# Optimization experiments

Hardware: AMD Instinct MI355X
Metric: run time of the kernel (lower is better)

## Reference

```python
import jax, jax.numpy as jnp
import numpy as np

N = 16384          # num nodes (128 graphs x 128 turbines)
E = 262144         # edges before self loops
TURBINE_NUM = 128
D_IN = 512         # input_dim (= 2*hidden_dim1)
H1 = 256           # hidden_dim1
H2 = 256           # hidden_dim2
NEG_SLOPE = 0.2    # PyG GATConv default leaky relu slope


def _glorot(key, shape, fan_in):
    return jax.random.normal(key, shape, dtype=jnp.float32) / np.sqrt(fan_in)


def setup_inputs() -> dict:
    key = jax.random.key(0)
    ks = jax.random.split(key, 12)
    x = jax.random.normal(ks[0], (N, H2), dtype=jnp.float32)
    adj = jax.random.randint(ks[1], (2, E), 0, N, dtype=jnp.int64)
    # fc: Linear(hidden_dim2 -> hidden_dim1); stored as [in, out]
    W_fc = _glorot(ks[2], (H2, H1), H2)
    b_fc = jnp.zeros((H1,), dtype=jnp.float32)
    # gat1: GATConv(H1 -> H1, heads=2, concat)
    W1 = _glorot(ks[3], (H1, 2 * H1), H1)
    a1_src = _glorot(ks[4], (2, H1), H1)
    a1_dst = _glorot(ks[5], (2, H1), H1)
    b1 = jnp.zeros((2 * H1,), dtype=jnp.float32)
    # gat2: GATConv(D_IN -> D_IN, heads=1, concat)
    W2 = _glorot(ks[6], (D_IN, D_IN), D_IN)
    a2_src = _glorot(ks[7], (1, D_IN), D_IN)
    a2_dst = _glorot(ks[8], (1, D_IN), D_IN)
    b2 = jnp.zeros((D_IN,), dtype=jnp.float32)
    return dict(x=x, adj=adj, W_fc=W_fc, b_fc=b_fc, W1=W1, a1_src=a1_src,
                a1_dst=a1_dst, b1=b1, W2=W2, a2_src=a2_src, a2_dst=a2_dst, b2=b2)


def gat_conv(x, src, dst, W, a_src, a_dst, bias, heads, out_ch):
    """PyG GATConv (eval mode, self loops already in src/dst)."""
    n = x.shape[0]
    h = (x @ W).reshape(n, heads, out_ch)                 # [N,H,C]
    al_s = jnp.einsum('nhc,hc->nh', h, a_src)             # [N,H]
    al_d = jnp.einsum('nhc,hc->nh', h, a_dst)
    e = jax.nn.leaky_relu(al_s[src] + al_d[dst], NEG_SLOPE)  # [E,H]
    # segment softmax over incoming edges per destination node
    e_max = jax.ops.segment_max(e, dst, num_segments=n)
    e_exp = jnp.exp(e - e_max[dst])
    denom = jax.ops.segment_sum(e_exp, dst, num_segments=n)
    alpha = e_exp / (denom[dst] + 1e-16)                  # [E,H]
    msg = h[src] * alpha[:, :, None]                      # [E,H,C]
    out = jax.ops.segment_sum(msg, dst, num_segments=n)   # [N,H,C]
    return out.reshape(n, heads * out_ch) + bias


def reference(x, adj, W_fc, b_fc, W1, a1_src, a1_dst, b1, W2, a2_src, a2_dst, b2):
    # add self loops (PyG GATConv default)
    loops = jnp.arange(N, dtype=adj.dtype)
    src = jnp.concatenate([adj[0], loops])
    dst = jnp.concatenate([adj[1], loops])
    h = jax.nn.relu(x @ W_fc + b_fc)                      # fc + ReLU
    h = gat_conv(h, src, dst, W1, a1_src, a1_dst, b1, heads=2, out_ch=H1)
    h = jax.nn.relu(h)
    h = gat_conv(h, src, dst, W2, a2_src, a2_dst, b2, heads=1, out_ch=D_IN)
    y = jax.nn.relu(h)
    return y.reshape(-1, TURBINE_NUM, y.shape[1])         # [128,128,512]
```

## Files before the change

kernel.cpp:

```cpp
#include <hip/hip_runtime.h>

#define N_NODES 16384
#define N_EDGES 262144
#define E_TOT   (N_EDGES + N_NODES)
#define NEG_SLOPE 0.2f

typedef __attribute__((ext_vector_type(8))) short short8;
typedef __attribute__((ext_vector_type(4))) float floatx4;
typedef __attribute__((ext_vector_type(2))) float floatx2;
typedef __attribute__((ext_vector_type(4))) int intx4;

__device__ __forceinline__ float bf2f(ushort u) {
    return __uint_as_float(((unsigned)u) << 16);
}
__device__ __forceinline__ ushort f2bf(float f) {
    unsigned u = __float_as_uint(f);
    u += 0x7fffu + ((u >> 16) & 1u);
    return (ushort)(u >> 16);
}
__device__ __forceinline__ float leaky(float x) {
    return x > 0.f ? x : NEG_SLOPE * x;
}

#define PREP_CAST   524288
#define PREP_T0     (PREP_CAST)
#define PREP_T1     (PREP_T0 + 65536)
#define PREP_T2     (PREP_T1 + 131072)
#define PREP_Z      (PREP_T2 + 262144)
#define PREP_TOT    (PREP_Z + 4096)

__global__ __launch_bounds__(256) void k_prep(const float* __restrict__ x,
                                              ushort* __restrict__ xb,
                                              const float* __restrict__ Wfc,
                                              ushort* __restrict__ WfcT,
                                              const float* __restrict__ W1,
                                              ushort* __restrict__ W1T,
                                              const float* __restrict__ W2,
                                              ushort* __restrict__ W2T,
                                              int* __restrict__ counts) {
    int idx = blockIdx.x * 256 + threadIdx.x;
    if (idx < PREP_CAST) {
        floatx4 v0 = *(const floatx4*)(x + (size_t)idx * 8);
        floatx4 v1 = *(const floatx4*)(x + (size_t)idx * 8 + 4);
        short8 r;
        r[0] = (short)f2bf(v0[0]); r[1] = (short)f2bf(v0[1]);
        r[2] = (short)f2bf(v0[2]); r[3] = (short)f2bf(v0[3]);
        r[4] = (short)f2bf(v1[0]); r[5] = (short)f2bf(v1[1]);
        r[6] = (short)f2bf(v1[2]); r[7] = (short)f2bf(v1[3]);
        *(short8*)(xb + (size_t)idx * 8) = r;
    } else if (idx < PREP_T1) {
        int t = idx - PREP_T0;
        int k = t >> 8, n = t & 255;
        WfcT[n * 256 + k] = f2bf(Wfc[t]);
    } else if (idx < PREP_T2) {
        int t = idx - PREP_T1;
        int k = t >> 9, n = t & 511;
        W1T[n * 256 + k] = f2bf(W1[t]);
    } else if (idx < PREP_Z) {
        int t = idx - PREP_T2;
        int k = t >> 9, n = t & 511;
        W2T[n * 512 + k] = f2bf(W2[t]);
    } else if (idx < PREP_TOT) {
        int t = idx - PREP_Z;
        *(intx4*)(counts + t * 4) = (intx4){0, 0, 0, 0};
    }
}

__global__ __launch_bounds__(256) void k_hist(const int* __restrict__ adj,
                                              int* __restrict__ counts) {
    int e = blockIdx.x * 256 + threadIdx.x;
    if (e < E_TOT) {
        int d = (e < N_EDGES) ? adj[N_EDGES + e] : (e - N_EDGES);
        atomicAdd(&counts[d], 1);
    }
}

__global__ __launch_bounds__(1024) void k_scan(const int* __restrict__ counts,
                                               int* __restrict__ offs,
                                               int* __restrict__ cursor) {
    __shared__ int part[1024];
    int t = threadIdx.x;
    int local[16];
    int sum = 0;
#pragma unroll
    for (int i = 0; i < 16; i++) {
        local[i] = sum;
        sum += counts[t * 16 + i];
    }
    part[t] = sum;
    __syncthreads();
    for (int d = 1; d < 1024; d <<= 1) {
        int v = (t >= d) ? part[t - d] : 0;
        __syncthreads();
        part[t] += v;
        __syncthreads();
    }
    int base = (t == 0) ? 0 : part[t - 1];
#pragma unroll
    for (int i = 0; i < 16; i++) {
        int o = base + local[i];
        offs[t * 16 + i] = o;
        cursor[t * 16 + i] = o;
    }
    if (t == 1023) offs[N_NODES] = part[1023];
}

__global__ __launch_bounds__(256) void k_scatter(const int* __restrict__ adj,
                                                 int* __restrict__ cursor,
                                                 int* __restrict__ esrc) {
    int e = blockIdx.x * 256 + threadIdx.x;
    if (e < E_TOT) {
        int s, d;
        if (e < N_EDGES) { s = adj[e]; d = adj[N_EDGES + e]; }
        else             { s = e - N_EDGES; d = s; }
        int pos = atomicAdd(&cursor[d], 1);
        esrc[pos] = s;
    }
}

#define BM 64
#define BN 64
#define BK 64
#define LDK (BK + 8)

__global__ __launch_bounds__(256) void gemm_bt(const ushort* __restrict__ A,
                                               const ushort* __restrict__ BT,
                                               const float* __restrict__ bias,
                                               ushort* __restrict__ C,
                                               int M, int Nc, int K, int relu) {
    __shared__ ushort As[BM * LDK];
    __shared__ ushort Bs[BN * LDK];
    int tid  = threadIdx.x;
    int wave = tid >> 6, lane = tid & 63;
    int quad = lane >> 4, l16 = lane & 15;
    int bm = blockIdx.x * BM, bn = blockIdx.y * BN;

    floatx4 acc[4];
#pragma unroll
    for (int j = 0; j < 4; j++) acc[j] = (floatx4){0.f, 0.f, 0.f, 0.f};

    int srow = tid >> 3;
    int skc  = (tid & 7) * 8;

    for (int kb = 0; kb < K; kb += BK) {
        const ushort* ga = A + (size_t)(bm + srow) * K + kb + skc;
        short8 a0 = *(const short8*)ga;
        short8 a1 = *(const short8*)(ga + (size_t)32 * K);
        const ushort* gb = BT + (size_t)(bn + srow) * K + kb + skc;
        short8 b0 = *(const short8*)gb;
        short8 b1 = *(const short8*)(gb + (size_t)32 * K);
        *(short8*)&As[srow * LDK + skc] = a0;
        *(short8*)&As[(srow + 32) * LDK + skc] = a1;
        *(short8*)&Bs[srow * LDK + skc] = b0;
        *(short8*)&Bs[(srow + 32) * LDK + skc] = b1;
        __syncthreads();

        int arow = wave * 16 + l16;
#pragma unroll
        for (int kk = 0; kk < BK; kk += 32) {
            short8 a = *(const short8*)&As[arow * LDK + kk + quad * 8];
#pragma unroll
            for (int j4 = 0; j4 < 4; j4++) {
                short8 b = *(const short8*)&Bs[(j4 * 16 + l16) * LDK + kk + quad * 8];
                acc[j4] = __builtin_amdgcn_mfma_f32_16x16x32_bf16(a, b, acc[j4], 0, 0, 0);
            }
        }
        __syncthreads();
    }

    int row = bm + wave * 16 + quad * 4;
#pragma unroll
    for (int j4 = 0; j4 < 4; j4++) {
        int col = bn + j4 * 16 + l16;
        float bv = bias ? bias[col] : 0.f;
#pragma unroll
        for (int i = 0; i < 4; i++) {
            float v = acc[j4][i] + bv;
            if (relu) v = fmaxf(v, 0.f);
            C[(size_t)(row + i) * Nc + col] = f2bf(v);
        }
    }
}

__global__ __launch_bounds__(256) void k_dots(const ushort* __restrict__ h,
                                              const float* __restrict__ asrc,
                                              const float* __restrict__ adst,
                                              float* __restrict__ als,
                                              float* __restrict__ ald,
                                              int heads) {
    int wave = threadIdx.x >> 6, lane = threadIdx.x & 63;
    int n = blockIdx.x * 4 + wave;
    const ushort* hr = h + (size_t)n * 512;
    int c = lane * 8;
    short8 hv = *(const short8*)(hr + c);
    floatx4 s0 = *(const floatx4*)(asrc + c);
    floatx4 s1 = *(const floatx4*)(asrc + c + 4);
    floatx4 d0 = *(const floatx4*)(adst + c);
    floatx4 d1 = *(const floatx4*)(adst + c + 4);
    float ps = 0.f, pd = 0.f;
#pragma unroll
    for (int j = 0; j < 4; j++) {
        float hf0 = bf2f((ushort)hv[j]);
        float hf1 = bf2f((ushort)hv[j + 4]);
        ps += hf0 * s0[j] + hf1 * s1[j];
        pd += hf0 * d0[j] + hf1 * d1[j];
    }
    int w = (heads == 2) ? 32 : 64;
    for (int m = 1; m < w; m <<= 1) {
        ps += __shfl_xor(ps, m, 64);
        pd += __shfl_xor(pd, m, 64);
    }
    if (heads == 2) {
        if (lane == 0)  { als[n * 2]     = ps; ald[n * 2]     = pd; }
        if (lane == 32) { als[n * 2 + 1] = ps; ald[n * 2 + 1] = pd; }
    } else {
        if (lane == 0)  { als[n] = ps; ald[n] = pd; }
    }
}

__global__ __launch_bounds__(256) void k_agg(const ushort* __restrict__ h,
                                             const float* __restrict__ als,
                                             const float* __restrict__ ald,
                                             const int* __restrict__ offs,
                                             const int* __restrict__ esrc,
                                             const float* __restrict__ bias,
                                             ushort* __restrict__ outb,
                                             float* __restrict__ outf,
                                             int heads) {
    int wave = threadIdx.x >> 6, lane = threadIdx.x & 63;
    int n = blockIdx.x * 4 + wave;
    int base = offs[n];
    int deg  = offs[n + 1] - base;

    int myhead = (heads == 2) ? (lane >> 5) : 0;
    int c = (heads == 2) ? (myhead * 256 + (lane & 31) * 8) : lane * 8;

    float aldh0 = ald[n * heads];
    float aldh1 = (heads == 2) ? ald[n * heads + 1] : 0.f;

    float m0 = -1e30f, m1 = -1e30f;
    for (int cb = 0; cb < deg; cb += 64) {
        int i = cb + lane;
        if (i < deg) {
            int s = esrc[base + i];
            m0 = fmaxf(m0, leaky(als[s * heads] + aldh0));
            if (heads == 2) m1 = fmaxf(m1, leaky(als[s * 2 + 1] + aldh1));
        }
    }
#pragma unroll
    for (int msk = 1; msk < 64; msk <<= 1) {
        m0 = fmaxf(m0, __shfl_xor(m0, msk, 64));
        m1 = fmaxf(m1, __shfl_xor(m1, msk, 64));
    }

    float s0 = 0.f, s1 = 0.f;
    for (int cb = 0; cb < deg; cb += 64) {
        int i = cb + lane;
        if (i < deg) {
            int s = esrc[base + i];
            s0 += __expf(leaky(als[s * heads] + aldh0) - m0);
            if (heads == 2) s1 += __expf(leaky(als[s * 2 + 1] + aldh1) - m1);
        }
    }
#pragma unroll
    for (int msk = 1; msk < 64; msk <<= 1) {
        s0 += __shfl_xor(s0, msk, 64);
        s1 += __shfl_xor(s1, msk, 64);
    }
    float inv0 = 1.f / (s0 + 1e-16f);
    float inv1 = 1.f / (s1 + 1e-16f);

    float acc[8];
#pragma unroll
    for (int q = 0; q < 8; q++) acc[q] = 0.f;
    const ushort* hc = h + c;

    for (int cb = 0; cb < deg; cb += 64) {
        int i = cb + lane;
        int sv = 0;
        float p0 = 0.f, p1 = 0.f;
        if (i < deg) {
            sv = esrc[base + i];
            p0 = __expf(leaky(als[sv * heads] + aldh0) - m0) * inv0;
            if (heads == 2) p1 = __expf(leaky(als[sv * 2 + 1] + aldh1) - m1) * inv1;
        }
        int cnt = min(64, deg - cb);
        for (int j = 0; j < cnt; j++) {
            int s   = __shfl(sv, j, 64);
            float a0 = __shfl(p0, j, 64);
            float a1 = __shfl(p1, j, 64);
            float al = myhead ? a1 : a0;
            short8 hv = *(const short8*)(hc + (size_t)s * 512);
#pragma unroll
            for (int q = 0; q < 8; q++) acc[q] += al * bf2f((ushort)hv[q]);
        }
    }

    float v[8];
#pragma unroll
    for (int q = 0; q < 8; q++) v[q] = fmaxf(acc[q] + bias[c + q], 0.f);
    if (outf) {
        float* op = outf + (size_t)n * 512 + c;
        *(floatx4*)op       = (floatx4){v[0], v[1], v[2], v[3]};
        *(floatx4*)(op + 4) = (floatx4){v[4], v[5], v[6], v[7]};
    } else {
        short8 r;
#pragma unroll
        for (int q = 0; q < 8; q++) r[q] = (short)f2bf(v[q]);
        *(short8*)(outb + (size_t)n * 512 + c) = r;
    }
}

extern "C" void kernel_launch(void* const* d_in, const int* in_sizes, int n_in,
                              void* d_out, int out_size, void* d_ws, size_t ws_size,
                              hipStream_t stream) {
    const float* x   = (const float*)d_in[0];
    const int*   adj = (const int*)d_in[1];
    const float* Wfc = (const float*)d_in[2];
    const float* bfc = (const float*)d_in[3];
    const float* W1  = (const float*)d_in[4];
    const float* a1s = (const float*)d_in[5];
    const float* a1d = (const float*)d_in[6];
    const float* b1  = (const float*)d_in[7];
    const float* W2  = (const float*)d_in[8];
    const float* a2s = (const float*)d_in[9];
    const float* a2d = (const float*)d_in[10];
    const float* b2  = (const float*)d_in[11];
    float* out = (float*)d_out;

    char* ws = (char*)d_ws;
    size_t off = 0;
    auto alloc = [&](size_t bytes) -> void* {
        void* p = ws + off;
        off += (bytes + 255) & ~(size_t)255;
        return p;
    };
    ushort* xb   = (ushort*)alloc((size_t)N_NODES * 256 * 2);
    ushort* h0b  = (ushort*)alloc((size_t)N_NODES * 256 * 2);
    ushort* h1b  = (ushort*)alloc((size_t)N_NODES * 512 * 2);
    ushort* g1b  = (ushort*)alloc((size_t)N_NODES * 512 * 2);
    int* counts  = (int*)alloc(N_NODES * 4);
    int* offs    = (int*)alloc((N_NODES + 1) * 4);
    int* cursor  = (int*)alloc(N_NODES * 4);
    int* esrc    = (int*)alloc(E_TOT * 4);
    ushort* WfcT = (ushort*)alloc(256 * 256 * 2);
    ushort* W1T  = (ushort*)alloc(512 * 256 * 2);
    ushort* W2T  = (ushort*)alloc(512 * 512 * 2);
    float* als1  = (float*)alloc(N_NODES * 2 * 4);
    float* ald1  = (float*)alloc(N_NODES * 2 * 4);
    float* als2  = (float*)alloc(N_NODES * 4);
    float* ald2  = (float*)alloc(N_NODES * 4);

    k_prep<<<PREP_TOT / 256, 256, 0, stream>>>(x, xb, Wfc, WfcT, W1, W1T, W2, W2T,
                                               counts);

    k_hist<<<(E_TOT + 255) / 256, 256, 0, stream>>>(adj, counts);
    k_scan<<<1, 1024, 0, stream>>>(counts, offs, cursor);
    k_scatter<<<(E_TOT + 255) / 256, 256, 0, stream>>>(adj, cursor, esrc);

    gemm_bt<<<dim3(N_NODES / BM, 256 / BN), 256, 0, stream>>>(xb, WfcT, bfc, h0b,
                                                              N_NODES, 256, 256, 1);
    gemm_bt<<<dim3(N_NODES / BM, 512 / BN), 256, 0, stream>>>(h0b, W1T, nullptr, h1b,
                                                              N_NODES, 512, 256, 0);
    k_dots<<<N_NODES / 4, 256, 0, stream>>>(h1b, a1s, a1d, als1, ald1, 2);
    k_agg<<<N_NODES / 4, 256, 0, stream>>>(h1b, als1, ald1, offs, esrc, b1,
                                           g1b, nullptr, 2);

    gemm_bt<<<dim3(N_NODES / BM, 512 / BN), 256, 0, stream>>>(g1b, W2T, nullptr, h1b,
                                                              N_NODES, 512, 512, 0);
    k_dots<<<N_NODES / 4, 256, 0, stream>>>(h1b, a2s, a2d, als2, ald2, 1);
    k_agg<<<N_NODES / 4, 256, 0, stream>>>(h1b, als2, ald2, offs, esrc, b2,
                                           nullptr, out, 1);
}
```

Before: 269.2 us.

## Use 128x128 GEMM tiles, wave-shuffle scan, and unroll aggregation gathers by four

The bf16 MFMA GEMM moves from 64x64 tiles with one 16-row strip per wave to 128x128 tiles with a 4x4 MFMA block per wave. This gives more reuse of LDS fragments and fewer global loads per FLOP, at the cost of more registers and fewer blocks. The single-block prefix scan replaces the shared-memory Hillis-Steele loop, which needed many syncthreads, with wave shuffles plus a small cross-wave pass. The aggregation inner loop is unrolled by four so that several neighbor-row gathers are in flight at once.

```diff
diff --git a/kernel.cpp b/kernel.cpp
--- a/kernel.cpp
+++ b/kernel.cpp
@@ -7,7 +7,6 @@
 
 typedef __attribute__((ext_vector_type(8))) short short8;
 typedef __attribute__((ext_vector_type(4))) float floatx4;
-typedef __attribute__((ext_vector_type(2))) float floatx2;
 typedef __attribute__((ext_vector_type(4))) int intx4;
 
 __device__ __forceinline__ float bf2f(ushort u) {
@@ -78,31 +77,41 @@
 __global__ __launch_bounds__(1024) void k_scan(const int* __restrict__ counts,
                                                int* __restrict__ offs,
                                                int* __restrict__ cursor) {
-    __shared__ int part[1024];
-    int t = threadIdx.x;
+    __shared__ int wsum[16];
+    int t = threadIdx.x, lane = t & 63, w = t >> 6;
     int local[16];
-    int sum = 0;
+    int tot = 0;
 #pragma unroll
     for (int i = 0; i < 16; i++) {
-        local[i] = sum;
-        sum += counts[t * 16 + i];
-    }
-    part[t] = sum;
+        local[i] = tot;
+        tot += counts[t * 16 + i];
+    }
+    int incl = tot;
+#pragma unroll
+    for (int d = 1; d < 64; d <<= 1) {
+        int v = __shfl_up(incl, d, 64);
+        if (lane >= d) incl += v;
+    }
+    if (lane == 63) wsum[w] = incl;
     __syncthreads();
-    for (int d = 1; d < 1024; d <<= 1) {
-        int v = (t >= d) ? part[t - d] : 0;
-        __syncthreads();
-        part[t] += v;
-        __syncthreads();
-    }
-    int base = (t == 0) ? 0 : part[t - 1];
+    if (w == 0) {
+        int v = (lane < 16) ? wsum[lane] : 0;
+#pragma unroll
+        for (int d = 1; d < 16; d <<= 1) {
+            int u = __shfl_up(v, d, 64);
+            if (lane >= d) v += u;
+        }
+        if (lane < 16) wsum[lane] = v;
+    }
+    __syncthreads();
+    int base = ((w == 0) ? 0 : wsum[w - 1]) + incl - tot;
 #pragma unroll
     for (int i = 0; i < 16; i++) {
         int o = base + local[i];
         offs[t * 16 + i] = o;
         cursor[t * 16 + i] = o;
     }
-    if (t == 1023) offs[N_NODES] = part[1023];
+    if (t == 1023) offs[N_NODES] = wsum[15];
 }
 
 __global__ __launch_bounds__(256) void k_scatter(const int* __restrict__ adj,
@@ -118,66 +127,80 @@
     }
 }
 
-#define BM 64
-#define BN 64
-#define BK 64
-#define LDK (BK + 8)
-
-__global__ __launch_bounds__(256) void gemm_bt(const ushort* __restrict__ A,
+#define GM 128
+#define GN 128
+#define GK 64
+#define LDK2 72
+
+__global__ __launch_bounds__(256) void gemm128(const ushort* __restrict__ A,
                                                const ushort* __restrict__ BT,
                                                const float* __restrict__ bias,
                                                ushort* __restrict__ C,
                                                int M, int Nc, int K, int relu) {
-    __shared__ ushort As[BM * LDK];
-    __shared__ ushort Bs[BN * LDK];
-    int tid  = threadIdx.x;
-    int wave = tid >> 6, lane = tid & 63;
+    __shared__ ushort As[GM * LDK2];
+    __shared__ ushort Bs[GN * LDK2];
+    int tid = threadIdx.x, wave = tid >> 6, lane = tid & 63;
     int quad = lane >> 4, l16 = lane & 15;
-    int bm = blockIdx.x * BM, bn = blockIdx.y * BN;
-
-    floatx4 acc[4];
-#pragma unroll
-    for (int j = 0; j < 4; j++) acc[j] = (floatx4){0.f, 0.f, 0.f, 0.f};
-
-    int srow = tid >> 3;
-    int skc  = (tid & 7) * 8;
-
-    for (int kb = 0; kb < K; kb += BK) {
-        const ushort* ga = A + (size_t)(bm + srow) * K + kb + skc;
-        short8 a0 = *(const short8*)ga;
-        short8 a1 = *(const short8*)(ga + (size_t)32 * K);
-        const ushort* gb = BT + (size_t)(bn + srow) * K + kb + skc;
-        short8 b0 = *(const short8*)gb;
-        short8 b1 = *(const short8*)(gb + (size_t)32 * K);
-        *(short8*)&As[srow * LDK + skc] = a0;
-        *(short8*)&As[(srow + 32) * LDK + skc] = a1;
-        *(short8*)&Bs[srow * LDK + skc] = b0;
-        *(short8*)&Bs[(srow + 32) * LDK + skc] = b1;
+    int bm = blockIdx.x * GM, bn = blockIdx.y * GN;
+    int wm = (wave & 1) * 64, wn = (wave >> 1) * 64;
+
+    floatx4 acc[4][4];
+#pragma unroll
+    for (int mi = 0; mi < 4; mi++)
+#pragma unroll
+        for (int ni = 0; ni < 4; ni++)
+            acc[mi][ni] = (floatx4){0.f, 0.f, 0.f, 0.f};
+
+    for (int kb = 0; kb < K; kb += GK) {
+        short8 av[4], bv[4];
+#pragma unroll
+        for (int t = 0; t < 4; t++) {
+            int ci = tid + 256 * t;
+            int row = ci >> 3, col = (ci & 7) * 8;
+            av[t] = *(const short8*)(A + (size_t)(bm + row) * K + kb + col);
+            bv[t] = *(const short8*)(BT + (size_t)(bn + row) * K + kb + col);
+        }
         __syncthreads();
-
-        int arow = wave * 16 + l16;
-#pragma unroll
-        for (int kk = 0; kk < BK; kk += 32) {
-            short8 a = *(const short8*)&As[arow * LDK + kk + quad * 8];
-#pragma unroll
-            for (int j4 = 0; j4 < 4; j4++) {
-                short8 b = *(const short8*)&Bs[(j4 * 16 + l16) * LDK + kk + quad * 8];
-                acc[j4] = __builtin_amdgcn_mfma_f32_16x16x32_bf16(a, b, acc[j4], 0, 0, 0);
+#pragma unroll
+        for (int t = 0; t < 4; t++) {
+            int ci = tid + 256 * t;
+            int row = ci >> 3, col = (ci & 7) * 8;
+            *(short8*)&As[row * LDK2 + col] = av[t];
+            *(short8*)&Bs[row * LDK2 + col] = bv[t];
+        }
+        __syncthreads();
+
+#pragma unroll
+        for (int kk = 0; kk < GK; kk += 32) {
+            short8 af[4], bf[4];
+#pragma unroll
+            for (int mi = 0; mi < 4; mi++)
+                af[mi] = *(const short8*)&As[(wm + mi * 16 + l16) * LDK2 + kk + quad * 8];
+#pragma unroll
+            for (int ni = 0; ni < 4; ni++)
+                bf[ni] = *(const short8*)&Bs[(wn + ni * 16 + l16) * LDK2 + kk + quad * 8];
+#pragma unroll
+            for (int mi = 0; mi < 4; mi++)
+#pragma unroll
+                for (int ni = 0; ni < 4; ni++)
+                    acc[mi][ni] = __builtin_amdgcn_mfma_f32_16x16x32_bf16(
+                        af[mi], bf[ni], acc[mi][ni], 0, 0, 0);
+        }
+    }
+
+#pragma unroll
+    for (int mi = 0; mi < 4; mi++) {
+        int row = bm + wm + mi * 16 + quad * 4;
+#pragma unroll
+        for (int ni = 0; ni < 4; ni++) {
+            int col = bn + wn + ni * 16 + l16;
+            float bv = bias ? bias[col] : 0.f;
+#pragma unroll
+            for (int i = 0; i < 4; i++) {
+                float v = acc[mi][ni][i] + bv;
+                if (relu) v = fmaxf(v, 0.f);
+                C[(size_t)(row + i) * Nc + col] = f2bf(v);
             }
-        }
-        __syncthreads();
-    }
-
-    int row = bm + wave * 16 + quad * 4;
-#pragma unroll
-    for (int j4 = 0; j4 < 4; j4++) {
-        int col = bn + j4 * 16 + l16;
-        float bv = bias ? bias[col] : 0.f;
-#pragma unroll
-        for (int i = 0; i < 4; i++) {
-            float v = acc[j4][i] + bv;
-            if (relu) v = fmaxf(v, 0.f);
-            C[(size_t)(row + i) * Nc + col] = f2bf(v);
         }
     }
 }
@@ -285,10 +308,35 @@
             if (heads == 2) p1 = __expf(leaky(als[sv * 2 + 1] + aldh1) - m1) * inv1;
         }
         int cnt = min(64, deg - cb);
-        for (int j = 0; j < cnt; j++) {
-            int s   = __shfl(sv, j, 64);
-            float a0 = __shfl(p0, j, 64);
-            float a1 = __shfl(p1, j, 64);
+        int j = 0;
+        for (; j + 4 <= cnt; j += 4) {
+            int sj0 = __shfl(sv, j, 64);
+            int sj1 = __shfl(sv, j + 1, 64);
+            int sj2 = __shfl(sv, j + 2, 64);
+            int sj3 = __shfl(sv, j + 3, 64);
+            float a00 = __shfl(p0, j, 64),     a01 = __shfl(p1, j, 64);
+            float a10 = __shfl(p0, j + 1, 64), a11 = __shfl(p1, j + 1, 64);
+            float a20 = __shfl(p0, j + 2, 64), a21 = __shfl(p1, j + 2, 64);
+            float a30 = __shfl(p0, j + 3, 64), a31 = __shfl(p1, j + 3, 64);
+            float al0 = myhead ? a01 : a00;
+            float al1 = myhead ? a11 : a10;
+            float al2 = myhead ? a21 : a20;
+            float al3 = myhead ? a31 : a30;
+            short8 h0v = *(const short8*)(hc + (size_t)sj0 * 512);
+            short8 h1v = *(const short8*)(hc + (size_t)sj1 * 512);
+            short8 h2v = *(const short8*)(hc + (size_t)sj2 * 512);
+            short8 h3v = *(const short8*)(hc + (size_t)sj3 * 512);
+#pragma unroll
+            for (int q = 0; q < 8; q++) {
+                acc[q] += al0 * bf2f((ushort)h0v[q]);
+                acc[q] += al1 * bf2f((ushort)h1v[q]);
+                acc[q] += al2 * bf2f((ushort)h2v[q]);
+                acc[q] += al3 * bf2f((ushort)h3v[q]);
+            }
+        }
+        for (; j < cnt; j++) {
+            int s = __shfl(sv, j, 64);
+            float a0 = __shfl(p0, j, 64), a1 = __shfl(p1, j, 64);
             float al = myhead ? a1 : a0;
             short8 hv = *(const short8*)(hc + (size_t)s * 512);
 #pragma unroll
@@ -358,15 +406,15 @@
     k_scan<<<1, 1024, 0, stream>>>(counts, offs, cursor);
     k_scatter<<<(E_TOT + 255) / 256, 256, 0, stream>>>(adj, cursor, esrc);
 
-    gemm_bt<<<dim3(N_NODES / BM, 256 / BN), 256, 0, stream>>>(xb, WfcT, bfc, h0b,
+    gemm128<<<dim3(N_NODES / GM, 256 / GN), 256, 0, stream>>>(xb, WfcT, bfc, h0b,
                                                               N_NODES, 256, 256, 1);
-    gemm_bt<<<dim3(N_NODES / BM, 512 / BN), 256, 0, stream>>>(h0b, W1T, nullptr, h1b,
+    gemm128<<<dim3(N_NODES / GM, 512 / GN), 256, 0, stream>>>(h0b, W1T, nullptr, h1b,
                                                               N_NODES, 512, 256, 0);
     k_dots<<<N_NODES / 4, 256, 0, stream>>>(h1b, a1s, a1d, als1, ald1, 2);
     k_agg<<<N_NODES / 4, 256, 0, stream>>>(h1b, als1, ald1, offs, esrc, b1,
                                            g1b, nullptr, 2);
 
-    gemm_bt<<<dim3(N_NODES / BM, 512 / BN), 256, 0, stream>>>(g1b, W2T, nullptr, h1b,
+    gemm128<<<dim3(N_NODES / GM, 512 / GN), 256, 0, stream>>>(g1b, W2T, nullptr, h1b,
                                                               N_NODES, 512, 512, 0);
     k_dots<<<N_NODES / 4, 256, 0, stream>>>(h1b, a2s, a2d, als2, ald2, 1);
     k_agg<<<N_NODES / 4, 256, 0, stream>>>(h1b, als2, ald2, offs, esrc, b2,
```

New measurement: 263.1 us. 1.02x faster.
